# Kernel optimization log

Hardware: AMD Instinct MI355X
Metric: run time of the kernel (lower is better)

The kernel has to match this reference:

```python
import jax, jax.numpy as jnp
import numpy as np

NUM_HEADS = 16


def rotary_pos_emb(x):
    # x: [b, h, s, d] with interleaved rotary pairs (d even)
    d, s = x.shape[-1], x.shape[-2]
    ts = jnp.arange(0, d, 2, dtype=jnp.float32)
    inv_freqs = 10000.0 ** (-ts / d)                      # [d/2]
    grid = jnp.arange(s, dtype=jnp.float32)[:, None] * inv_freqs[None, :]  # [s, d/2]
    sin = jnp.repeat(jnp.sin(grid), 2, axis=-1)           # [s, d]
    cos = jnp.repeat(jnp.cos(grid), 2, axis=-1)           # [s, d]
    x1, x2 = x[..., ::2], x[..., 1::2]
    xs = jnp.stack([-x2, x1], axis=-1).reshape(x.shape)   # rotate pairs
    return x * cos + xs * sin


def setup_inputs() -> dict:
    key = jax.random.key(0)
    ks = jax.random.split(key, 6)
    b, l, d = 2, 2048, 1024
    x = jax.random.normal(ks[0], (b, l, d), dtype=jnp.float32)
    # additive causal mask: 0 on/below diag, large negative above
    causal = jnp.tril(jnp.ones((l, l), dtype=bool))
    mask = jnp.where(causal, 0.0, -1e9).astype(jnp.float32)[None, None]  # [1,1,l,l]
    s = 0.01  # VarianceScaling(0.01)-ish small init
    Wq = jax.random.normal(ks[1], (d, d), dtype=jnp.float32) * s
    Wk = jax.random.normal(ks[2], (d, d), dtype=jnp.float32) * s
    Wv = jax.random.normal(ks[3], (d, d), dtype=jnp.float32) * s
    Wo = jax.random.normal(ks[4], (d, d), dtype=jnp.float32) * s
    return {"x": x, "mask": mask, "Wq": Wq, "Wk": Wk, "Wv": Wv, "Wo": Wo}


def reference(x, mask, Wq, Wk, Wv, Wo):
    b, l, d = x.shape
    h = NUM_HEADS
    k_sz = d // h
    split = lambda t: t.reshape(b, l, h, k_sz).transpose(0, 2, 1, 3)  # b h l k
    # NOTE: original scales q by 1/sqrt(model_dim) (not key_size), before RoPE
    q = split(x @ Wq / jnp.sqrt(jnp.float32(d)))
    q = rotary_pos_emb(q)
    k = rotary_pos_emb(split(x @ Wk))
    v = split(x @ Wv)
    logits = jnp.einsum('bhik,bhjk->bhij', q, k) + mask   # [b,h,l,l]
    a = jax.nn.softmax(logits, axis=-1)
    y = jnp.einsum('bhij,bhjv->bhiv', a, v)               # [b,h,l,k]
    y = y.transpose(0, 2, 1, 3).reshape(b, l, d)
    return y @ Wo
```

## Files before the change

### kernel.cpp

```cpp
#include <hip/hip_runtime.h>
#include <math.h>

#define L 2048
#define D 1024
#define H 16
#define KS 64
#define BBATCH 2

typedef float f32x4 __attribute__((ext_vector_type(4)));
typedef short s16x8 __attribute__((ext_vector_type(8)));

__device__ __forceinline__ ushort f2bf(float f) {
    union { float f; unsigned u; } v; v.f = f;
    unsigned lsb = (v.u >> 16) & 1u;
    v.u += 0x7fffu + lsb;
    return (ushort)(v.u >> 16);
}

__device__ __forceinline__ unsigned fbits(float f) {
    union { float f; unsigned u; } v; v.f = f; return v.u;
}

__device__ __forceinline__ void gl_lds16(const ushort* g, ushort* l) {
    __builtin_amdgcn_global_load_lds(
        (const __attribute__((address_space(1))) unsigned int*)g,
        (__attribute__((address_space(3))) unsigned int*)l, 16, 0, 0);
}

__global__ __launch_bounds__(256)
void prep(const float* __restrict__ x,
          const float* __restrict__ W0, const float* __restrict__ W1,
          const float* __restrict__ W2, const float* __restrict__ W3,
          ushort* __restrict__ xb, ushort* __restrict__ Wt,
          float2* __restrict__ tab)
{
    __shared__ float T[32][33];
    const int bid = blockIdx.x;
    const int tid = threadIdx.x;
    if (bid < 4096) {
        const int i = bid * 1024 + tid * 4;
        const float4 v = *(const float4*)&x[i];
        ushort4 p = make_ushort4(f2bf(v.x), f2bf(v.y), f2bf(v.z), f2bf(v.w));
        *(ushort4*)&xb[i] = p;
    } else if (bid < 8192) {
        const int t = bid - 4096;
        const int z = t >> 10;
        const float* W = (z == 0) ? W0 : (z == 1) ? W1 : (z == 2) ? W2 : W3;
        ushort* out = Wt + (size_t)z * D * D;
        const int r0 = ((t >> 5) & 31) * 32, c0 = (t & 31) * 32;
        const int tr = tid >> 3, tc = (tid & 7) * 4;
        const float4 v = *(const float4*)&W[(size_t)(r0 + tr) * D + c0 + tc];
        T[tr][tc + 0] = v.x; T[tr][tc + 1] = v.y;
        T[tr][tc + 2] = v.z; T[tr][tc + 3] = v.w;
        __syncthreads();
        ushort4 p = make_ushort4(f2bf(T[tc + 0][tr]), f2bf(T[tc + 1][tr]),
                                 f2bf(T[tc + 2][tr]), f2bf(T[tc + 3][tr]));
        *(ushort4*)&out[(size_t)(c0 + tr) * D + r0 + tc] = p;
    } else {
        const int idx = (bid - 8192) * 256 + tid;
        const int dd2 = idx >> 11, s = idx & 2047;
        const float inv = __expf(-(float)(2 * dd2) * (9.210340371976184f / 64.0f));
        float sn, cs;
        sincosf((float)s * inv, &sn, &cs);
        tab[idx] = make_float2(cs, sn);
    }
}

__global__ __launch_bounds__(256)
void qkv_gemm(const ushort* __restrict__ A, const ushort* __restrict__ B,
              const float2* __restrict__ tab,
              ushort* __restrict__ Qo, ushort* __restrict__ Ko,
              ushort* __restrict__ Vto)
{
    __shared__ __align__(16) ushort smem[18432];
    ushort* As = smem;
    ushort* Bs = smem + 4096;

    const int tid  = threadIdx.x;
    const int wv   = tid >> 6, lane = tid & 63;
    const int i16  = lane & 15, quad = lane >> 4;
    const int wr   = wv >> 1, wc = wv & 1;
    const int m0   = blockIdx.y * 128;
    const int n0   = blockIdx.x * 128;

    f32x4 acc[4][4];
    #pragma unroll
    for (int i = 0; i < 4; ++i)
        #pragma unroll
        for (int j = 0; j < 4; ++j) acc[i][j] = (f32x4){0.f, 0.f, 0.f, 0.f};

    for (int k0 = 0; k0 < D; k0 += 32) {
        __syncthreads();
        {
            int c = wv * 64 + lane;
            gl_lds16(A + (size_t)(m0 + (c >> 2)) * D + k0 + (c & 3) * 8,
                     As + (size_t)(wv * 64) * 8);
            c = 256 + wv * 64 + lane;
            gl_lds16(A + (size_t)(m0 + (c >> 2)) * D + k0 + (c & 3) * 8,
                     As + (size_t)(256 + wv * 64) * 8);
        }
        {
            int c = wv * 64 + lane;
            gl_lds16(B + (size_t)(n0 + (c >> 2)) * D + k0 + (c & 3) * 8,
                     Bs + (size_t)(wv * 64) * 8);
            c = 256 + wv * 64 + lane;
            gl_lds16(B + (size_t)(n0 + (c >> 2)) * D + k0 + (c & 3) * 8,
                     Bs + (size_t)(256 + wv * 64) * 8);
        }
        __syncthreads();
        s16x8 af[4], bf[4];
        #pragma unroll
        for (int mt = 0; mt < 4; ++mt)
            af[mt] = *(const s16x8*)&As[(wr * 64 + mt * 16 + i16) * 32 + quad * 8];
        #pragma unroll
        for (int nt = 0; nt < 4; ++nt)
            bf[nt] = *(const s16x8*)&Bs[(wc * 64 + nt * 16 + i16) * 32 + quad * 8];
        #pragma unroll
        for (int mt = 0; mt < 4; ++mt)
            #pragma unroll
            for (int nt = 0; nt < 4; ++nt)
                acc[mt][nt] = __builtin_amdgcn_mfma_f32_16x16x32_bf16(
                    af[mt], bf[nt], acc[mt][nt], 0, 0, 0);
    }

    __syncthreads();
    ushort* T = smem + wv * 4608;

    if (m0 < 2048) {
        const bool isQ = (m0 < 1024);
        ushort* out = isQ ? Qo : Ko;
        const int mb = isQ ? m0 : (m0 - 1024);
        const int s0 = ((n0 + wc * 64) & 2047);
        #pragma unroll
        for (int mt = 0; mt < 4; ++mt) {
            const int dd = mt * 16 + quad * 4;
            #pragma unroll
            for (int nt = 0; nt < 4; ++nt) {
                const int lt = nt * 16 + i16;
                const int s = s0 + lt;
                ushort4 p;
                #pragma unroll
                for (int pr = 0; pr < 2; ++pr) {
                    float e = acc[mt][nt][2 * pr];
                    float o = acc[mt][nt][2 * pr + 1];
                    if (isQ) { e *= 0.03125f; o *= 0.03125f; }
                    const float2 cssn = tab[(size_t)((dd >> 1) + pr) * 2048 + s];
                    const float ne = e * cssn.x - o * cssn.y;
                    const float no = o * cssn.x + e * cssn.y;
                    if (pr == 0) { p.x = f2bf(ne); p.y = f2bf(no); }
                    else         { p.z = f2bf(ne); p.w = f2bf(no); }
                }
                *(ushort4*)&T[lt * 72 + dd] = p;
            }
        }
        __builtin_amdgcn_s_waitcnt(0);
        const int hh = (mb + wr * 64) >> 6;
        const int tok0 = n0 + wc * 64;
        const int b = tok0 >> 11;
        const int dl = (lane & 7) * 8;
        #pragma unroll
        for (int c = 0; c < 8; ++c) {
            const int tl = c * 8 + (lane >> 3);
            const s16x8 val = *(const s16x8*)&T[tl * 72 + dl];
            *(s16x8*)&out[((size_t)(b * H + hh) * L + (s0 + tl)) * KS + dl] = val;
        }
    } else {
        const int vbase = (m0 - 2048) + wr * 64;
        const int tbase = n0 + wc * 64;
        #pragma unroll
        for (int mt = 0; mt < 4; ++mt)
            #pragma unroll
            for (int nt = 0; nt < 4; ++nt) {
                const int tl = nt * 16 + i16;
                #pragma unroll
                for (int r = 0; r < 4; ++r)
                    T[(mt * 16 + quad * 4 + r) * 72 + tl] = f2bf(acc[mt][nt][r]);
            }
        __builtin_amdgcn_s_waitcnt(0);
        const int tl0 = (lane & 7) * 8;
        #pragma unroll
        for (int c = 0; c < 8; ++c) {
            const int vl = c * 8 + (lane >> 3);
            const s16x8 val = *(const s16x8*)&T[vl * 72 + tl0];
            const int vdim = vbase + vl;
            const int hh = vdim >> 6, dd = vdim & 63;
            const int token0 = tbase + tl0;
            const int b = token0 >> 11, sv = token0 & 2047;
            *(s16x8*)&Vto[((size_t)(b * H + hh) * KS + dd) * L + sv] = val;
        }
    }
}

__global__ __launch_bounds__(256)
void oproj_gemm(const ushort* __restrict__ A, const ushort* __restrict__ B,
                float* __restrict__ out)
{
    __shared__ __align__(16) ushort As[128 * 32];
    __shared__ __align__(16) ushort Bs[64 * 32];
    const int tid  = threadIdx.x;
    const int wv   = tid >> 6, lane = tid & 63;
    const int i16  = lane & 15, quad = lane >> 4;
    const int wr   = wv >> 1, wc = wv & 1;
    const int m0   = blockIdx.y * 128;
    const int n0   = blockIdx.x * 64;

    f32x4 acc[4][2];
    #pragma unroll
    for (int i = 0; i < 4; ++i)
        #pragma unroll
        for (int j = 0; j < 2; ++j) acc[i][j] = (f32x4){0.f, 0.f, 0.f, 0.f};

    for (int k0 = 0; k0 < D; k0 += 32) {
        __syncthreads();
        {
            int c = wv * 64 + lane;
            gl_lds16(A + (size_t)(m0 + (c >> 2)) * D + k0 + (c & 3) * 8,
                     As + (size_t)(wv * 64) * 8);
            c = 256 + wv * 64 + lane;
            gl_lds16(A + (size_t)(m0 + (c >> 2)) * D + k0 + (c & 3) * 8,
                     As + (size_t)(256 + wv * 64) * 8);
        }
        {
            int c = wv * 64 + lane;
            gl_lds16(B + (size_t)(n0 + (c >> 2)) * D + k0 + (c & 3) * 8,
                     Bs + (size_t)(wv * 64) * 8);
        }
        __syncthreads();
        s16x8 af[4], bf[2];
        #pragma unroll
        for (int mt = 0; mt < 4; ++mt)
            af[mt] = *(const s16x8*)&As[(wr * 64 + mt * 16 + i16) * 32 + quad * 8];
        #pragma unroll
        for (int nt = 0; nt < 2; ++nt)
            bf[nt] = *(const s16x8*)&Bs[(wc * 32 + nt * 16 + i16) * 32 + quad * 8];
        #pragma unroll
        for (int mt = 0; mt < 4; ++mt)
            #pragma unroll
            for (int nt = 0; nt < 2; ++nt)
                acc[mt][nt] = __builtin_amdgcn_mfma_f32_16x16x32_bf16(
                    af[mt], bf[nt], acc[mt][nt], 0, 0, 0);
    }

    #pragma unroll
    for (int mt = 0; mt < 4; ++mt)
        #pragma unroll
        for (int nt = 0; nt < 2; ++nt) {
            const int od = n0 + wc * 32 + nt * 16 + i16;
            const int tk = m0 + wr * 64 + mt * 16 + quad * 4;
            #pragma unroll
            for (int r = 0; r < 4; ++r)
                out[(size_t)(tk + r) * D + od] = acc[mt][nt][r];
        }
}

__global__ __launch_bounds__(512)
void attn_mfma(const ushort* __restrict__ Q, const ushort* __restrict__ K,
               const ushort* __restrict__ Vt, ushort* __restrict__ Yb)
{
    const int bh   = blockIdx.y;
    const int qa   = blockIdx.x;
    const int qb   = 31 - qa;
    const int tid  = threadIdx.x;
    const int wave = tid >> 6, lane = tid & 63;
    const int half = wave >> 2, wv4 = wave & 3;
    const int i16  = lane & 15, quad = lane >> 4;
    const int qt   = half ? qb : qa;
    const int r0   = qt * 64 + wv4 * 16;
    const int row  = r0 + i16;

    __shared__ ushort Ks[64 * 72];
    __shared__ ushort Vs[64 * 72];
    __shared__ ushort Ps[8][16 * 72];

    const ushort* Qb = Q  + (size_t)bh * L * KS;
    const ushort* Kb = K  + (size_t)bh * L * KS;
    const ushort* Vb = Vt + (size_t)bh * KS * L;

    const s16x8 qf0 = *(const s16x8*)(Qb + (size_t)row * KS + quad * 8);
    const s16x8 qf1 = *(const s16x8*)(Qb + (size_t)row * KS + 32 + quad * 8);

    const int sr = tid >> 3, sseg = (tid & 7) * 8;
    s16x8 kpre = *(const s16x8*)(Kb + (size_t)sr * KS + sseg);
    s16x8 vpre = *(const s16x8*)(Vb + (size_t)sr * L + sseg);
    *(s16x8*)&Ks[sr * 72 + sseg] = kpre;
    *(s16x8*)&Vs[sr * 72 + sseg] = vpre;
    __syncthreads();

    f32x4 O0 = {0.f,0.f,0.f,0.f}, O1 = O0, O2 = O0, O3 = O0;
    float psum = 0.0f;

    for (int jt = 0; jt <= qb; ++jt) {
        const int j0 = jt * 64;
        const bool has_next = (jt < qb);

        if (has_next) {
            const int j0n = j0 + 64;
            kpre = *(const s16x8*)(Kb + (size_t)(j0n + sr) * KS + sseg);
            vpre = *(const s16x8*)(Vb + (size_t)sr * L + j0n + sseg);
        }

        if (jt <= qt) {
            f32x4 st[4];
            #pragma unroll
            for (int nt = 0; nt < 4; ++nt) {
                const s16x8 kf0 = *(const s16x8*)&Ks[(nt * 16 + i16) * 72 + quad * 8];
                const s16x8 kf1 = *(const s16x8*)&Ks[(nt * 16 + i16) * 72 + 32 + quad * 8];
                f32x4 c = {0.f,0.f,0.f,0.f};
                c = __builtin_amdgcn_mfma_f32_16x16x32_bf16(kf0, qf0, c, 0, 0, 0);
                c = __builtin_amdgcn_mfma_f32_16x16x32_bf16(kf1, qf1, c, 0, 0, 0);
                st[nt] = c;
            }
            if (jt == qt) {
                #pragma unroll
                for (int nt = 0; nt < 4; ++nt)
                    #pragma unroll
                    for (int rg = 0; rg < 4; ++rg) {
                        const int j = j0 + nt * 16 + quad * 4 + rg;
                        if (j > row) st[nt][rg] = -1e30f;
                    }
            }
            float pv[4][4];
            #pragma unroll
            for (int nt = 0; nt < 4; ++nt)
                #pragma unroll
                for (int rg = 0; rg < 4; ++rg) {
                    pv[nt][rg] = __expf(st[nt][rg]);
                    psum += pv[nt][rg];
                }
            ushort* P2 = &Ps[wave][0];
            #pragma unroll
            for (int nt = 0; nt < 4; ++nt) {
                uint2 pk;
                pk.x = __builtin_amdgcn_perm(fbits(pv[nt][1]), fbits(pv[nt][0]), 0x07060302u);
                pk.y = __builtin_amdgcn_perm(fbits(pv[nt][3]), fbits(pv[nt][2]), 0x07060302u);
                *(uint2*)(P2 + i16 * 72 + nt * 16 + quad * 4) = pk;
            }
            const s16x8 pf0 = *(const s16x8*)(P2 + i16 * 72 + quad * 8);
            const s16x8 pf1 = *(const s16x8*)(P2 + i16 * 72 + 32 + quad * 8);
            s16x8 v0, v1;
            v0 = *(const s16x8*)&Vs[(0 * 16 + i16) * 72 + quad * 8];
            v1 = *(const s16x8*)&Vs[(0 * 16 + i16) * 72 + 32 + quad * 8];
            O0 = __builtin_amdgcn_mfma_f32_16x16x32_bf16(v0, pf0, O0, 0, 0, 0);
            O0 = __builtin_amdgcn_mfma_f32_16x16x32_bf16(v1, pf1, O0, 0, 0, 0);
            v0 = *(const s16x8*)&Vs[(1 * 16 + i16) * 72 + quad * 8];
            v1 = *(const s16x8*)&Vs[(1 * 16 + i16) * 72 + 32 + quad * 8];
            O1 = __builtin_amdgcn_mfma_f32_16x16x32_bf16(v0, pf0, O1, 0, 0, 0);
            O1 = __builtin_amdgcn_mfma_f32_16x16x32_bf16(v1, pf1, O1, 0, 0, 0);
            v0 = *(const s16x8*)&Vs[(2 * 16 + i16) * 72 + quad * 8];
            v1 = *(const s16x8*)&Vs[(2 * 16 + i16) * 72 + 32 + quad * 8];
            O2 = __builtin_amdgcn_mfma_f32_16x16x32_bf16(v0, pf0, O2, 0, 0, 0);
            O2 = __builtin_amdgcn_mfma_f32_16x16x32_bf16(v1, pf1, O2, 0, 0, 0);
            v0 = *(const s16x8*)&Vs[(3 * 16 + i16) * 72 + quad * 8];
            v1 = *(const s16x8*)&Vs[(3 * 16 + i16) * 72 + 32 + quad * 8];
            O3 = __builtin_amdgcn_mfma_f32_16x16x32_bf16(v0, pf0, O3, 0, 0, 0);
            O3 = __builtin_amdgcn_mfma_f32_16x16x32_bf16(v1, pf1, O3, 0, 0, 0);
        }

        __syncthreads();
        if (has_next) {
            *(s16x8*)&Ks[sr * 72 + sseg] = kpre;
            *(s16x8*)&Vs[sr * 72 + sseg] = vpre;
        }
        __syncthreads();
    }

    psum += __shfl_xor(psum, 16);
    psum += __shfl_xor(psum, 32);
    const float inv_l = __builtin_amdgcn_rcpf(psum);
    const int b = bh >> 4, hh = bh & 15;
    ushort* Yp = Yb + ((size_t)(b * L + row)) * D + hh * KS + quad * 4;
    f32x4 r;
    r = O0 * inv_l; *(ushort4*)(Yp +  0) = make_ushort4(f2bf(r[0]),f2bf(r[1]),f2bf(r[2]),f2bf(r[3]));
    r = O1 * inv_l; *(ushort4*)(Yp + 16) = make_ushort4(f2bf(r[0]),f2bf(r[1]),f2bf(r[2]),f2bf(r[3]));
    r = O2 * inv_l; *(ushort4*)(Yp + 32) = make_ushort4(f2bf(r[0]),f2bf(r[1]),f2bf(r[2]),f2bf(r[3]));
    r = O3 * inv_l; *(ushort4*)(Yp + 48) = make_ushort4(f2bf(r[0]),f2bf(r[1]),f2bf(r[2]),f2bf(r[3]));
}

extern "C" void kernel_launch(void* const* d_in, const int* in_sizes, int n_in,
                              void* d_out, int out_size, void* d_ws, size_t ws_size,
                              hipStream_t stream)
{
    const float* x  = (const float*)d_in[0];
    const float* Wq = (const float*)d_in[2];
    const float* Wk = (const float*)d_in[3];
    const float* Wv = (const float*)d_in[4];
    const float* Wo = (const float*)d_in[5];

    const size_t NTOK = (size_t)BBATCH * L;
    const size_t SZ   = NTOK * D;
    ushort* xb  = (ushort*)d_ws;
    ushort* Wt  = xb + SZ;
    ushort* Qb  = Wt + 4 * (size_t)D * D;
    ushort* Kb  = Qb + SZ;
    ushort* Vtb = Kb + SZ;
    ushort* Yb  = Vtb + SZ;
    float2* tab = (float2*)Yb;

    prep<<<dim3(8448), dim3(256), 0, stream>>>(x, Wq, Wk, Wv, Wo, xb, Wt, tab);

    qkv_gemm<<<dim3(32, 24), dim3(256), 0, stream>>>(Wt, xb, tab, Qb, Kb, Vtb);

    attn_mfma<<<dim3(16, 32), dim3(512), 0, stream>>>(Qb, Kb, Vtb, Yb);

    oproj_gemm<<<dim3(16, 32), dim3(256), 0, stream>>>(Yb, Wt + 3 * (size_t)D * D,
                                                       (float*)d_out);
}
```

Before: 200.7 us.

## Double-buffer K/V tiles in attention and write Q/K directly from registers

```diff
diff --git a/kernel.cpp b/kernel.cpp
--- a/kernel.cpp
+++ b/kernel.cpp
@@ -123,21 +123,18 @@
                     af[mt], bf[nt], acc[mt][nt], 0, 0, 0);
     }
 
-    __syncthreads();
-    ushort* T = smem + wv * 4608;
-
     if (m0 < 2048) {
         const bool isQ = (m0 < 1024);
         ushort* out = isQ ? Qo : Ko;
         const int mb = isQ ? m0 : (m0 - 1024);
-        const int s0 = ((n0 + wc * 64) & 2047);
-        #pragma unroll
-        for (int mt = 0; mt < 4; ++mt) {
-            const int dd = mt * 16 + quad * 4;
+        #pragma unroll
+        for (int mt = 0; mt < 4; ++mt)
             #pragma unroll
             for (int nt = 0; nt < 4; ++nt) {
-                const int lt = nt * 16 + i16;
-                const int s = s0 + lt;
+                const int token = n0 + wc * 64 + nt * 16 + i16;
+                const int b = token >> 11, s = token & 2047;
+                const int dim = mb + wr * 64 + mt * 16 + quad * 4;
+                const int hh = dim >> 6, dd = dim & 63;
                 ushort4 p;
                 #pragma unroll
                 for (int pr = 0; pr < 2; ++pr) {
@@ -150,21 +147,11 @@
                     if (pr == 0) { p.x = f2bf(ne); p.y = f2bf(no); }
                     else         { p.z = f2bf(ne); p.w = f2bf(no); }
                 }
-                *(ushort4*)&T[lt * 72 + dd] = p;
-            }
-        }
-        __builtin_amdgcn_s_waitcnt(0);
-        const int hh = (mb + wr * 64) >> 6;
-        const int tok0 = n0 + wc * 64;
-        const int b = tok0 >> 11;
-        const int dl = (lane & 7) * 8;
-        #pragma unroll
-        for (int c = 0; c < 8; ++c) {
-            const int tl = c * 8 + (lane >> 3);
-            const s16x8 val = *(const s16x8*)&T[tl * 72 + dl];
-            *(s16x8*)&out[((size_t)(b * H + hh) * L + (s0 + tl)) * KS + dl] = val;
-        }
+                *(ushort4*)&out[((size_t)(b * H + hh) * L + s) * KS + dd] = p;
+            }
     } else {
+        __syncthreads();
+        ushort* T = smem + wv * 4608;
         const int vbase = (m0 - 2048) + wr * 64;
         const int tbase = n0 + wc * 64;
         #pragma unroll
@@ -185,8 +172,8 @@
             const int vdim = vbase + vl;
             const int hh = vdim >> 6, dd = vdim & 63;
             const int token0 = tbase + tl0;
-            const int b = token0 >> 11, sv = token0 & 2047;
-            *(s16x8*)&Vto[((size_t)(b * H + hh) * KS + dd) * L + sv] = val;
+            const int b = token0 >> 11, s0 = token0 & 2047;
+            *(s16x8*)&Vto[((size_t)(b * H + hh) * KS + dd) * L + s0] = val;
         }
     }
 }
@@ -268,8 +255,8 @@
     const int r0   = qt * 64 + wv4 * 16;
     const int row  = r0 + i16;
 
-    __shared__ ushort Ks[64 * 72];
-    __shared__ ushort Vs[64 * 72];
+    __shared__ ushort Ks[2][64 * 72];
+    __shared__ ushort Vs[2][64 * 72];
     __shared__ ushort Ps[8][16 * 72];
 
     const ushort* Qb = Q  + (size_t)bh * L * KS;
@@ -282,29 +269,32 @@
     const int sr = tid >> 3, sseg = (tid & 7) * 8;
     s16x8 kpre = *(const s16x8*)(Kb + (size_t)sr * KS + sseg);
     s16x8 vpre = *(const s16x8*)(Vb + (size_t)sr * L + sseg);
-    *(s16x8*)&Ks[sr * 72 + sseg] = kpre;
-    *(s16x8*)&Vs[sr * 72 + sseg] = vpre;
+    *(s16x8*)&Ks[0][sr * 72 + sseg] = kpre;
+    *(s16x8*)&Vs[0][sr * 72 + sseg] = vpre;
     __syncthreads();
 
     f32x4 O0 = {0.f,0.f,0.f,0.f}, O1 = O0, O2 = O0, O3 = O0;
     float psum = 0.0f;
 
     for (int jt = 0; jt <= qb; ++jt) {
-        const int j0 = jt * 64;
+        const int cur = jt & 1;
         const bool has_next = (jt < qb);
 
         if (has_next) {
-            const int j0n = j0 + 64;
+            const int j0n = (jt + 1) * 64;
             kpre = *(const s16x8*)(Kb + (size_t)(j0n + sr) * KS + sseg);
             vpre = *(const s16x8*)(Vb + (size_t)sr * L + j0n + sseg);
         }
 
         if (jt <= qt) {
+            const int j0 = jt * 64;
+            const ushort* Ksb = &Ks[cur][0];
+            const ushort* Vsb = &Vs[cur][0];
             f32x4 st[4];
             #pragma unroll
             for (int nt = 0; nt < 4; ++nt) {
-                const s16x8 kf0 = *(const s16x8*)&Ks[(nt * 16 + i16) * 72 + quad * 8];
-                const s16x8 kf1 = *(const s16x8*)&Ks[(nt * 16 + i16) * 72 + 32 + quad * 8];
+                const s16x8 kf0 = *(const s16x8*)&Ksb[(nt * 16 + i16) * 72 + quad * 8];
+                const s16x8 kf1 = *(const s16x8*)&Ksb[(nt * 16 + i16) * 72 + 32 + quad * 8];
                 f32x4 c = {0.f,0.f,0.f,0.f};
                 c = __builtin_amdgcn_mfma_f32_16x16x32_bf16(kf0, qf0, c, 0, 0, 0);
                 c = __builtin_amdgcn_mfma_f32_16x16x32_bf16(kf1, qf1, c, 0, 0, 0);
@@ -338,30 +328,29 @@
             const s16x8 pf0 = *(const s16x8*)(P2 + i16 * 72 + quad * 8);
             const s16x8 pf1 = *(const s16x8*)(P2 + i16 * 72 + 32 + quad * 8);
             s16x8 v0, v1;
-            v0 = *(const s16x8*)&Vs[(0 * 16 + i16) * 72 + quad * 8];
-            v1 = *(const s16x8*)&Vs[(0 * 16 + i16) * 72 + 32 + quad * 8];
+            v0 = *(const s16x8*)&Vsb[(0 * 16 + i16) * 72 + quad * 8];
+            v1 = *(const s16x8*)&Vsb[(0 * 16 + i16) * 72 + 32 + quad * 8];
             O0 = __builtin_amdgcn_mfma_f32_16x16x32_bf16(v0, pf0, O0, 0, 0, 0);
             O0 = __builtin_amdgcn_mfma_f32_16x16x32_bf16(v1, pf1, O0, 0, 0, 0);
-            v0 = *(const s16x8*)&Vs[(1 * 16 + i16) * 72 + quad * 8];
-            v1 = *(const s16x8*)&Vs[(1 * 16 + i16) * 72 + 32 + quad * 8];
+            v0 = *(const s16x8*)&Vsb[(1 * 16 + i16) * 72 + quad * 8];
+            v1 = *(const s16x8*)&Vsb[(1 * 16 + i16) * 72 + 32 + quad * 8];
             O1 = __builtin_amdgcn_mfma_f32_16x16x32_bf16(v0, pf0, O1, 0, 0, 0);
             O1 = __builtin_amdgcn_mfma_f32_16x16x32_bf16(v1, pf1, O1, 0, 0, 0);
-            v0 = *(const s16x8*)&Vs[(2 * 16 + i16) * 72 + quad * 8];
-            v1 = *(const s16x8*)&Vs[(2 * 16 + i16) * 72 + 32 + quad * 8];
+            v0 = *(const s16x8*)&Vsb[(2 * 16 + i16) * 72 + quad * 8];
+            v1 = *(const s16x8*)&Vsb[(2 * 16 + i16) * 72 + 32 + quad * 8];
             O2 = __builtin_amdgcn_mfma_f32_16x16x32_bf16(v0, pf0, O2, 0, 0, 0);
             O2 = __builtin_amdgcn_mfma_f32_16x16x32_bf16(v1, pf1, O2, 0, 0, 0);
-            v0 = *(const s16x8*)&Vs[(3 * 16 + i16) * 72 + quad * 8];
-            v1 = *(const s16x8*)&Vs[(3 * 16 + i16) * 72 + 32 + quad * 8];
+            v0 = *(const s16x8*)&Vsb[(3 * 16 + i16) * 72 + quad * 8];
+            v1 = *(const s16x8*)&Vsb[(3 * 16 + i16) * 72 + 32 + quad * 8];
             O3 = __builtin_amdgcn_mfma_f32_16x16x32_bf16(v0, pf0, O3, 0, 0, 0);
             O3 = __builtin_amdgcn_mfma_f32_16x16x32_bf16(v1, pf1, O3, 0, 0, 0);
         }
 
-        __syncthreads();
         if (has_next) {
-            *(s16x8*)&Ks[sr * 72 + sseg] = kpre;
-            *(s16x8*)&Vs[sr * 72 + sseg] = vpre;
-        }
-        __syncthreads();
+            *(s16x8*)&Ks[cur ^ 1][sr * 72 + sseg] = kpre;
+            *(s16x8*)&Vs[cur ^ 1][sr * 72 + sseg] = vpre;
+            __syncthreads();
+        }
     }
 
     psum += __shfl_xor(psum, 16);
```

After: 200.9 us. Within noise of the previous version (+0.1%).
